# Performance work log

Measured on AMD Instinct MI355X. Metric: run time of the kernel, lower is better.

The kernel has to match this reference:

```python
import jax, jax.numpy as jnp
import numpy as np

EPS = 1e-5


def setup_inputs() -> dict:
    key = jax.random.key(0)
    k1, k2, k3 = jax.random.split(key, 3)
    x = jax.random.normal(k1, (16384, 1024), dtype=jnp.float32)
    weight = jax.random.normal(k2, (1024, 1024), dtype=jnp.float32)  # [out, in]
    bias = jax.random.normal(k3, (1024,), dtype=jnp.float32)
    return {"x": x, "weight": weight, "bias": bias}


def reference(x, weight, bias):
    # activation_quant_real: per-row int8 symmetric quantization
    act_scale = 127.0 / jnp.clip(jnp.max(jnp.abs(x), axis=-1, keepdims=True), EPS)  # [T,1]
    qx = jnp.clip(jnp.round(x * act_scale), -128.0, 127.0)  # int8 values held in f32

    # weight_quant_real: per-tensor ternary (int2) quantization
    w_scale = 1.0 / jnp.clip(jnp.mean(jnp.abs(weight)), EPS)  # scalar
    qw = jnp.clip(jnp.round(weight * w_scale), -1.0, 1.0)  # {-1,0,1}

    acc = jnp.einsum("tk,nk->tn", qx, qw)  # [T, out]

    # fused dequant: out = acc / act_scale / w_scale + bias
    out = acc / act_scale / w_scale + bias
    return out
```

## Files before the change

kernel.cpp:

```cpp
#include <hip/hip_runtime.h>
#include <stdint.h>

#define EPS 1e-5f
#define T_DIM 16384
#define N_DIM 1024
#define K_DIM 1024


typedef int v4i __attribute__((ext_vector_type(4)));

__global__ __launch_bounds__(256) void k_xq_wabs(
    const float* __restrict__ x, const float* __restrict__ w,
    char* __restrict__ qx, float* __restrict__ dq, double* __restrict__ part) {
    const int bid = blockIdx.x;
    const int tid = threadIdx.x;

    if (bid < 4096) {
        const int row  = bid * 4 + (tid >> 6);
        const int lane = tid & 63;
        const float4* xr = (const float4*)(x + (long)row * K_DIM);
        float4 v[4];
#pragma unroll
        for (int i = 0; i < 4; ++i) v[i] = xr[i * 64 + lane];
        float m = 0.0f;
#pragma unroll
        for (int i = 0; i < 4; ++i)
            m = fmaxf(m, fmaxf(fmaxf(fabsf(v[i].x), fabsf(v[i].y)),
                               fmaxf(fabsf(v[i].z), fabsf(v[i].w))));
#pragma unroll
        for (int s = 32; s > 0; s >>= 1) m = fmaxf(m, __shfl_xor(m, s));
        m = fmaxf(m, EPS);
        if (lane == 0) dq[row] = m * (1.0f / 127.0f);
        const float s = 127.0f / m;
        int* qrow = (int*)(qx + (long)row * K_DIM);
#pragma unroll
        for (int i = 0; i < 4; ++i) {
            float f0 = fminf(fmaxf(rintf(v[i].x * s), -128.f), 127.f);
            float f1 = fminf(fmaxf(rintf(v[i].y * s), -128.f), 127.f);
            float f2 = fminf(fmaxf(rintf(v[i].z * s), -128.f), 127.f);
            float f3 = fminf(fmaxf(rintf(v[i].w * s), -128.f), 127.f);
            int q0 = (int)f0, q1 = (int)f1, q2 = (int)f2, q3 = (int)f3;
            qrow[i * 64 + lane] = (q0 & 255) | ((q1 & 255) << 8) |
                                  ((q2 & 255) << 16) | ((q3 & 255) << 24);
        }
    } else {
        const int wb = bid - 4096;
        const int base = wb * 256 + tid;
        const float4* w4 = (const float4*)w;
        double sum = 0.0;
#pragma unroll
        for (int i = 0; i < 4; ++i) {
            float4 v = w4[base + i * 65536];
            sum += (double)fabsf(v.x) + (double)fabsf(v.y) +
                   (double)fabsf(v.z) + (double)fabsf(v.w);
        }
        __shared__ double redd[256];
        redd[tid] = sum;
        __syncthreads();
#pragma unroll
        for (int st = 128; st > 0; st >>= 1) {
            if (tid < st) redd[tid] += redd[tid + st];
            __syncthreads();
        }
        if (tid == 0) part[wb] = redd[0];
    }
}

__global__ __launch_bounds__(256) void k_wquant(
    const float* __restrict__ w, char* __restrict__ qw,
    const double* __restrict__ part, float* __restrict__ meanf) {
    const int tid = threadIdx.x;
    __shared__ double red[256];
    red[tid] = part[tid];
    __syncthreads();
#pragma unroll
    for (int st = 128; st > 0; st >>= 1) {
        if (tid < st) red[tid] += red[tid + st];
        __syncthreads();
    }
    const double mean = fmax(red[0] / 1048576.0, (double)EPS);
    if (blockIdx.x == 0 && tid == 0) meanf[0] = (float)mean;
    const double ws = 1.0 / mean;
    const long i = (long)blockIdx.x * 256 + tid;
    float4 v = ((const float4*)w)[i];
    int q0 = (int)rint((double)v.x * ws);
    int q1 = (int)rint((double)v.y * ws);
    int q2 = (int)rint((double)v.z * ws);
    int q3 = (int)rint((double)v.w * ws);
    q0 = max(-1, min(1, q0)); q1 = max(-1, min(1, q1));
    q2 = max(-1, min(1, q2)); q3 = max(-1, min(1, q3));
    int packed = (q0 & 255) | ((q1 & 255) << 8) | ((q2 & 255) << 16) | ((q3 & 255) << 24);
    ((int*)qw)[i] = packed;
}

#define BM 256
#define BN 256
#define BK 128

__device__ __forceinline__ void gld_lds16(const void* g, void* l) {
    __builtin_amdgcn_global_load_lds(
        (const __attribute__((address_space(1))) void*)g,
        (__attribute__((address_space(3))) void*)l, 16, 0, 0);
}

__global__ __launch_bounds__(512, 2) void k_gemm(
    const char* __restrict__ qx, const char* __restrict__ qw,
    const float* __restrict__ dq, const float* __restrict__ meanf_p,
    const float* __restrict__ bias, float* __restrict__ out) {
    __shared__ __attribute__((aligned(16))) char As[2][BM * BK];
    __shared__ __attribute__((aligned(16))) char Bs[2][BN * BK];

    const int tid  = threadIdx.x;
    const int lane = tid & 63;
    const int wid  = tid >> 6;
    const int wr   = wid >> 2;
    const int wc   = wid & 3;

    const int bid  = blockIdx.x;
    const int work = (bid & 7) * 32 + (bid >> 3);
    const int brow = work >> 2;
    const int bcol = work & 3;
    const long arow0 = (long)brow * BM;
    const int  ncol0 = bcol * BN;

    int s_row[4], s_src[4], s_off[4];
#pragma unroll
    for (int p = 0; p < 4; ++p) {
        int off = tid * 16 + p * 8192;
        int row = off >> 7;
        int ch  = (off >> 4) & 7;
        int sch = ch ^ (row & 7);
        s_row[p] = row; s_src[p] = sch * 16; s_off[p] = off;
    }

#define STAGE(k0_, buf_)                                                      \
    {                                                                         \
        _Pragma("unroll")                                                     \
        for (int p = 0; p < 4; ++p) {                                         \
            const char* gA = qx + ((arow0 + s_row[p]) << 10) + (k0_) + s_src[p]; \
            gld_lds16(gA, As[buf_] + s_off[p]);                               \
            const char* gB = qw + (((long)(ncol0 + s_row[p])) << 10) + (k0_) + s_src[p]; \
            gld_lds16(gB, Bs[buf_] + s_off[p]);                               \
        }                                                                     \
    }

    v4i acc[8][4] = {};

    const int r15 = lane & 15;
    const int cg  = lane >> 4;
    const int sw  = lane & 7;

    STAGE(0, 0);
    __syncthreads();

#pragma unroll
    for (int k0 = 0; k0 < 8; ++k0) {
        const int cur = k0 & 1;
        if (k0 < 7) STAGE((k0 + 1) * BK, cur ^ 1);

#pragma unroll
        for (int ks = 0; ks < 2; ++ks) {
            const int c = ks * 4 + cg;
            const int rch = (c ^ sw) * 16;
            v4i a[8], b[4];
#pragma unroll
            for (int m = 0; m < 8; ++m) {
                int row = wr * 128 + m * 16 + r15;
                a[m] = *(const v4i*)(As[cur] + row * BK + rch);
            }
#pragma unroll
            for (int n = 0; n < 4; ++n) {
                int row = wc * 64 + n * 16 + r15;
                b[n] = *(const v4i*)(Bs[cur] + row * BK + rch);
            }
#pragma unroll
            for (int m = 0; m < 8; ++m)
#pragma unroll
                for (int n = 0; n < 4; ++n)
                    acc[m][n] = __builtin_amdgcn_mfma_i32_16x16x64_i8(
                        a[m], b[n], acc[m][n], 0, 0, 0);
        }
        __syncthreads();
    }

    const float wmean = meanf_p[0];
    const int ocol = ncol0 + wc * 64 + r15;
    float bv[4];
#pragma unroll
    for (int n = 0; n < 4; ++n) bv[n] = bias[ocol + n * 16];
#pragma unroll
    for (int m = 0; m < 8; ++m) {
#pragma unroll
        for (int rr = 0; rr < 4; ++rr) {
            long orow = arow0 + wr * 128 + m * 16 + cg * 4 + rr;
            float d = dq[orow] * wmean;
#pragma unroll
            for (int n = 0; n < 4; ++n)
                out[orow * N_DIM + ocol + n * 16] = (float)acc[m][n][rr] * d + bv[n];
        }
    }
}

extern "C" void kernel_launch(void* const* d_in, const int* in_sizes, int n_in,
                              void* d_out, int out_size, void* d_ws, size_t ws_size,
                              hipStream_t stream) {
    (void)in_sizes; (void)n_in; (void)out_size; (void)ws_size;
    const float* x    = (const float*)d_in[0];
    const float* w    = (const float*)d_in[1];
    const float* bias = (const float*)d_in[2];
    float* out = (float*)d_out;

    char*   ws    = (char*)d_ws;
    char*   qx    = ws;
    char*   qw    = ws + 16777216;
    float*  dq    = (float*)(ws + 17825792);
    double* part  = (double*)(ws + 17891328);
    float*  meanf = (float*)(ws + 17893376);

    k_xq_wabs<<<dim3(4096 + 256), dim3(256), 0, stream>>>(x, w, qx, dq, part);
    k_wquant <<<dim3(1024),       dim3(256), 0, stream>>>(w, qw, part, meanf);
    k_gemm   <<<dim3(256),        dim3(512), 0, stream>>>(qx, qw, dq, meanf, bias, out);
}
```

Measured before the change: 44.93 us.

## Split GEMM tile into two 128-column halves and swizzle quant row order

The GEMM block now covers its 256 output columns as two sequential 128-wide halves. The accumulator is halved to 4x4 per wave, which lowers register pressure and may allow more occupancy, and the first half's epilogue stores overlap with prefetching the second half's B tile. The price is reloading the A tile from global or L2 twice per block and running one extra pipeline fill. The activation-quant kernel also remaps block-to-row order with an XCD-style swizzle.

```diff
diff --git a/kernel.cpp b/kernel.cpp
--- a/kernel.cpp
+++ b/kernel.cpp
@@ -16,7 +16,8 @@
     const int tid = threadIdx.x;
 
     if (bid < 4096) {
-        const int row  = bid * 4 + (tid >> 6);
+        const int rb   = (bid & 7) * 512 + (bid >> 3);
+        const int row  = rb * 4 + (tid >> 6);
         const int lane = tid & 63;
         const float4* xr = (const float4*)(x + (long)row * K_DIM);
         float4 v[4];
@@ -94,7 +95,7 @@
 }
 
 #define BM 256
-#define BN 256
+#define BN 128
 #define BK 128
 
 __device__ __forceinline__ void gld_lds16(const void* g, void* l) {
@@ -113,15 +114,15 @@
     const int tid  = threadIdx.x;
     const int lane = tid & 63;
     const int wid  = tid >> 6;
-    const int wr   = wid >> 2;
-    const int wc   = wid & 3;
+    const int wr   = wid >> 1;
+    const int wc   = wid & 1;
 
     const int bid  = blockIdx.x;
     const int work = (bid & 7) * 32 + (bid >> 3);
     const int brow = work >> 2;
-    const int bcol = work & 3;
+    const int bcp  = work & 3;
     const long arow0 = (long)brow * BM;
-    const int  ncol0 = bcol * BN;
+    const int  ncol0 = bcp * 256;
 
     int s_row[4], s_src[4], s_off[4];
 #pragma unroll
@@ -129,76 +130,104 @@
         int off = tid * 16 + p * 8192;
         int row = off >> 7;
         int ch  = (off >> 4) & 7;
-        int sch = ch ^ (row & 7);
-        s_row[p] = row; s_src[p] = sch * 16; s_off[p] = off;
-    }
-
-#define STAGE(k0_, buf_)                                                      \
+        s_row[p] = row; s_src[p] = (ch ^ (row & 7)) * 16; s_off[p] = off;
+    }
+
+#define STAGE(k0_, buf_, nc_)                                                 \
     {                                                                         \
         _Pragma("unroll")                                                     \
         for (int p = 0; p < 4; ++p) {                                         \
             const char* gA = qx + ((arow0 + s_row[p]) << 10) + (k0_) + s_src[p]; \
             gld_lds16(gA, As[buf_] + s_off[p]);                               \
-            const char* gB = qw + (((long)(ncol0 + s_row[p])) << 10) + (k0_) + s_src[p]; \
+        }                                                                     \
+        _Pragma("unroll")                                                     \
+        for (int p = 0; p < 2; ++p) {                                         \
+            const char* gB = qw + (((long)((nc_) + s_row[p])) << 10) + (k0_) + s_src[p]; \
             gld_lds16(gB, Bs[buf_] + s_off[p]);                               \
         }                                                                     \
     }
 
-    v4i acc[8][4] = {};
+    v4i acc[4][4] = {};
 
     const int r15 = lane & 15;
     const int cg  = lane >> 4;
     const int sw  = lane & 7;
 
-    STAGE(0, 0);
+#define COMPUTE(cur_)                                                         \
+    {                                                                         \
+        _Pragma("unroll")                                                     \
+        for (int ks = 0; ks < 2; ++ks) {                                      \
+            const int c   = ks * 4 + cg;                                      \
+            const int rch = (c ^ sw) * 16;                                    \
+            v4i a[4], b[4];                                                   \
+            _Pragma("unroll")                                                 \
+            for (int m = 0; m < 4; ++m) {                                     \
+                int row = wr * 64 + m * 16 + r15;                             \
+                a[m] = *(const v4i*)(As[cur_] + row * BK + rch);              \
+            }                                                                 \
+            _Pragma("unroll")                                                 \
+            for (int n = 0; n < 4; ++n) {                                     \
+                int row = wc * 64 + n * 16 + r15;                             \
+                b[n] = *(const v4i*)(Bs[cur_] + row * BK + rch);              \
+            }                                                                 \
+            _Pragma("unroll")                                                 \
+            for (int m = 0; m < 4; ++m)                                       \
+                _Pragma("unroll")                                             \
+                for (int n = 0; n < 4; ++n)                                   \
+                    acc[m][n] = __builtin_amdgcn_mfma_i32_16x16x64_i8(        \
+                        a[m], b[n], acc[m][n], 0, 0, 0);                      \
+        }                                                                     \
+    }
+
+#define EPI(nc_)                                                              \
+    {                                                                         \
+        const int ocol = (nc_) + wc * 64 + r15;                               \
+        float bv[4];                                                          \
+        _Pragma("unroll")                                                     \
+        for (int n = 0; n < 4; ++n) bv[n] = bias[ocol + n * 16];              \
+        _Pragma("unroll")                                                     \
+        for (int m = 0; m < 4; ++m) {                                         \
+            _Pragma("unroll")                                                 \
+            for (int rr = 0; rr < 4; ++rr) {                                  \
+                long orow = arow0 + wr * 64 + m * 16 + cg * 4 + rr;           \
+                float d = dq[orow] * wmean;                                   \
+                _Pragma("unroll")                                             \
+                for (int n = 0; n < 4; ++n)                                   \
+                    out[orow * N_DIM + ocol + n * 16] =                       \
+                        (float)acc[m][n][rr] * d + bv[n];                     \
+            }                                                                 \
+        }                                                                     \
+    }
+
+    const float wmean = meanf_p[0];
+
+    STAGE(0, 0, ncol0);
     __syncthreads();
 
 #pragma unroll
     for (int k0 = 0; k0 < 8; ++k0) {
         const int cur = k0 & 1;
-        if (k0 < 7) STAGE((k0 + 1) * BK, cur ^ 1);
-
-#pragma unroll
-        for (int ks = 0; ks < 2; ++ks) {
-            const int c = ks * 4 + cg;
-            const int rch = (c ^ sw) * 16;
-            v4i a[8], b[4];
-#pragma unroll
-            for (int m = 0; m < 8; ++m) {
-                int row = wr * 128 + m * 16 + r15;
-                a[m] = *(const v4i*)(As[cur] + row * BK + rch);
-            }
-#pragma unroll
-            for (int n = 0; n < 4; ++n) {
-                int row = wc * 64 + n * 16 + r15;
-                b[n] = *(const v4i*)(Bs[cur] + row * BK + rch);
-            }
-#pragma unroll
-            for (int m = 0; m < 8; ++m)
-#pragma unroll
-                for (int n = 0; n < 4; ++n)
-                    acc[m][n] = __builtin_amdgcn_mfma_i32_16x16x64_i8(
-                        a[m], b[n], acc[m][n], 0, 0, 0);
-        }
-        __syncthreads();
-    }
-
-    const float wmean = meanf_p[0];
-    const int ocol = ncol0 + wc * 64 + r15;
-    float bv[4];
-#pragma unroll
-    for (int n = 0; n < 4; ++n) bv[n] = bias[ocol + n * 16];
-#pragma unroll
-    for (int m = 0; m < 8; ++m) {
-#pragma unroll
-        for (int rr = 0; rr < 4; ++rr) {
-            long orow = arow0 + wr * 128 + m * 16 + cg * 4 + rr;
-            float d = dq[orow] * wmean;
-#pragma unroll
-            for (int n = 0; n < 4; ++n)
-                out[orow * N_DIM + ocol + n * 16] = (float)acc[m][n][rr] * d + bv[n];
-        }
-    }
+        if (k0 < 7) STAGE((k0 + 1) * BK, cur ^ 1, ncol0)
+        else        STAGE(0,             cur ^ 1, ncol0 + 128);
+        COMPUTE(cur);
+        __syncthreads();
+    }
+
+    EPI(ncol0);
+#pragma unroll
+    for (int m = 0; m < 4; ++m)
+#pragma unroll
+        for (int n = 0; n < 4; ++n) acc[m][n] = (v4i)(0);
+
+#pragma unroll
+    for (int k0 = 0; k0 < 8; ++k0) {
+        const int cur = k0 & 1;
+        if (k0 < 7) STAGE((k0 + 1) * BK, cur ^ 1, ncol0 + 128);
+        COMPUTE(cur);
+        __syncthreads();
+    }
+
+    EPI(ncol0 + 128);
 }
 
 extern "C" void kernel_launch(void* const* d_in, const int* in_sizes, int n_in,
```

New measurement: 51.14 us. 1.14x slower.

## Switch GEMM to 4-buffer BK=64 pipeline with split staging and setprio

Applied to the files above, without the earlier changes.

The GEMM K tile shrinks to 64 and uses a four-deep LDS ring with prefetch distance two. The A and B global-to-LDS loads are split and interleaved between two MFMA halves, synchronised with explicit vmcnt waits and raw barriers instead of full syncthreads. s_setprio is raised around the MFMA bursts. The quantization kernel also remaps row blocks in an interleaved order. This aims to overlap memory with compute and cut barrier stalls, but it adds more barriers per K step and relies on delicate vmcnt counting.

```diff
diff --git a/kernel.cpp b/kernel.cpp
--- a/kernel.cpp
+++ b/kernel.cpp
@@ -16,7 +16,8 @@
     const int tid = threadIdx.x;
 
     if (bid < 4096) {
-        const int row  = bid * 4 + (tid >> 6);
+        const int rb   = (bid & 7) * 512 + (bid >> 3);
+        const int row  = rb * 4 + (tid >> 6);
         const int lane = tid & 63;
         const float4* xr = (const float4*)(x + (long)row * K_DIM);
         float4 v[4];
@@ -95,7 +96,8 @@
 
 #define BM 256
 #define BN 256
-#define BK 128
+#define BK 64
+#define TILE_B (BM * BK)
 
 __device__ __forceinline__ void gld_lds16(const void* g, void* l) {
     __builtin_amdgcn_global_load_lds(
@@ -107,8 +109,8 @@
     const char* __restrict__ qx, const char* __restrict__ qw,
     const float* __restrict__ dq, const float* __restrict__ meanf_p,
     const float* __restrict__ bias, float* __restrict__ out) {
-    __shared__ __attribute__((aligned(16))) char As[2][BM * BK];
-    __shared__ __attribute__((aligned(16))) char Bs[2][BN * BK];
+    __shared__ __attribute__((aligned(16))) char As[4][TILE_B];
+    __shared__ __attribute__((aligned(16))) char Bs[4][TILE_B];
 
     const int tid  = threadIdx.x;
     const int lane = tid & 63;
@@ -123,24 +125,29 @@
     const long arow0 = (long)brow * BM;
     const int  ncol0 = bcol * BN;
 
-    int s_row[4], s_src[4], s_off[4];
-#pragma unroll
-    for (int p = 0; p < 4; ++p) {
+    int s_row[2], s_src[2], s_off[2];
+#pragma unroll
+    for (int p = 0; p < 2; ++p) {
         int off = tid * 16 + p * 8192;
-        int row = off >> 7;
-        int ch  = (off >> 4) & 7;
-        int sch = ch ^ (row & 7);
-        s_row[p] = row; s_src[p] = sch * 16; s_off[p] = off;
-    }
-
-#define STAGE(k0_, buf_)                                                      \
+        int row = off >> 6;
+        int ch  = (off >> 4) & 3;
+        s_row[p] = row; s_src[p] = (ch ^ (row & 3)) * 16; s_off[p] = off;
+    }
+
+#define STAGE_A(kt_, buf_)                                                    \
     {                                                                         \
         _Pragma("unroll")                                                     \
-        for (int p = 0; p < 4; ++p) {                                         \
-            const char* gA = qx + ((arow0 + s_row[p]) << 10) + (k0_) + s_src[p]; \
-            gld_lds16(gA, As[buf_] + s_off[p]);                               \
-            const char* gB = qw + (((long)(ncol0 + s_row[p])) << 10) + (k0_) + s_src[p]; \
-            gld_lds16(gB, Bs[buf_] + s_off[p]);                               \
+        for (int p = 0; p < 2; ++p) {                                         \
+            const char* g = qx + ((arow0 + s_row[p]) << 10) + (kt_) * 64 + s_src[p]; \
+            gld_lds16(g, As[buf_] + s_off[p]);                                \
+        }                                                                     \
+    }
+#define STAGE_B(kt_, buf_)                                                    \
+    {                                                                         \
+        _Pragma("unroll")                                                     \
+        for (int p = 0; p < 2; ++p) {                                         \
+            const char* g = qw + (((long)(ncol0 + s_row[p])) << 10) + (kt_) * 64 + s_src[p]; \
+            gld_lds16(g, Bs[buf_] + s_off[p]);                                \
         }                                                                     \
     }
 
@@ -148,39 +155,56 @@
 
     const int r15 = lane & 15;
     const int cg  = lane >> 4;
-    const int sw  = lane & 7;
-
-    STAGE(0, 0);
-    __syncthreads();
-
-#pragma unroll
-    for (int k0 = 0; k0 < 8; ++k0) {
-        const int cur = k0 & 1;
-        if (k0 < 7) STAGE((k0 + 1) * BK, cur ^ 1);
-
-#pragma unroll
-        for (int ks = 0; ks < 2; ++ks) {
-            const int c = ks * 4 + cg;
-            const int rch = (c ^ sw) * 16;
-            v4i a[8], b[4];
-#pragma unroll
-            for (int m = 0; m < 8; ++m) {
-                int row = wr * 128 + m * 16 + r15;
-                a[m] = *(const v4i*)(As[cur] + row * BK + rch);
-            }
-#pragma unroll
-            for (int n = 0; n < 4; ++n) {
-                int row = wc * 64 + n * 16 + r15;
-                b[n] = *(const v4i*)(Bs[cur] + row * BK + rch);
-            }
-#pragma unroll
-            for (int m = 0; m < 8; ++m)
-#pragma unroll
-                for (int n = 0; n < 4; ++n)
-                    acc[m][n] = __builtin_amdgcn_mfma_i32_16x16x64_i8(
-                        a[m], b[n], acc[m][n], 0, 0, 0);
-        }
-        __syncthreads();
+    const int rch = ((cg ^ (r15 & 3)) & 3) * 16;
+
+    STAGE_A(0, 0); STAGE_B(0, 0);
+    STAGE_A(1, 1); STAGE_B(1, 1);
+    asm volatile("s_waitcnt vmcnt(4)" ::: "memory");
+    __builtin_amdgcn_s_barrier();
+
+#pragma unroll
+    for (int t = 0; t < 16; ++t) {
+        const int cur = t & 3;
+        const char* Ab = As[cur];
+        const char* Bb = Bs[cur];
+
+        v4i a[4], b[4];
+#pragma unroll
+        for (int n = 0; n < 4; ++n)
+            b[n] = *(const v4i*)(Bb + (wc * 64 + n * 16 + r15) * BK + rch);
+#pragma unroll
+        for (int m = 0; m < 4; ++m)
+            a[m] = *(const v4i*)(Ab + (wr * 128 + m * 16 + r15) * BK + rch);
+        if (t < 14) STAGE_A(t + 2, (t + 2) & 3);
+        __builtin_amdgcn_s_setprio(1);
+#pragma unroll
+        for (int m = 0; m < 4; ++m)
+#pragma unroll
+            for (int n = 0; n < 4; ++n)
+                acc[m][n] = __builtin_amdgcn_mfma_i32_16x16x64_i8(
+                    a[m], b[n], acc[m][n], 0, 0, 0);
+        __builtin_amdgcn_s_setprio(0);
+
+#pragma unroll
+        for (int m = 0; m < 4; ++m)
+            a[m] = *(const v4i*)(Ab + (wr * 128 + (m + 4) * 16 + r15) * BK + rch);
+        if (t < 14) STAGE_B(t + 2, (t + 2) & 3);
+        __builtin_amdgcn_s_setprio(1);
+#pragma unroll
+        for (int m = 0; m < 4; ++m)
+#pragma unroll
+            for (int n = 0; n < 4; ++n)
+                acc[m + 4][n] = __builtin_amdgcn_mfma_i32_16x16x64_i8(
+                    a[m], b[n], acc[m + 4][n], 0, 0, 0);
+        __builtin_amdgcn_s_setprio(0);
+
+        if (t < 14) {
+            asm volatile("s_waitcnt vmcnt(4)" ::: "memory");
+            __builtin_amdgcn_s_barrier();
+        } else if (t == 14) {
+            asm volatile("s_waitcnt vmcnt(0)" ::: "memory");
+            __builtin_amdgcn_s_barrier();
+        }
     }
 
     const float wmean = meanf_p[0];
```

Measured after the change: 46.77 us. 4.1% more time.
